# Performance work log

Hardware: AMD Instinct MI355X
Metric: run time of the kernel (lower is better)

## Reference

```python
import jax, jax.numpy as jnp
import numpy as np

EPS = 1e-05
FACT = 2.0
REJECT_RATIO = 1.0


def setup_inputs() -> dict:
    key = jax.random.key(0)
    k1, k2 = jax.random.split(key)
    B, N = 8, 4096
    pc1 = jax.random.normal(k1, (B, 4, N), dtype=jnp.float32)
    pc2 = jax.random.normal(k2, (B, 4, N), dtype=jnp.float32)
    # homogeneous coordinates: last row = 1
    pc1 = pc1.at[:, 3, :].set(1.0)
    pc2 = pc2.at[:, 3, :].set(1.0)
    return {"pc1": pc1, "pc2": pc2}


def _rot_to_quat(R):
    # standard rotation-matrix -> quaternion (w, x, y, z)
    r00, r11, r22 = R[0, 0], R[1, 1], R[2, 2]
    qw = 0.5 * jnp.sqrt(jnp.maximum(1e-12, 1.0 + r00 + r11 + r22))
    qx = 0.5 * jnp.sqrt(jnp.maximum(0.0, 1.0 + r00 - r11 - r22))
    qy = 0.5 * jnp.sqrt(jnp.maximum(0.0, 1.0 - r00 + r11 - r22))
    qz = 0.5 * jnp.sqrt(jnp.maximum(0.0, 1.0 - r00 - r11 + r22))
    qx = jnp.where(R[2, 1] - R[1, 2] < 0, -qx, qx)
    qy = jnp.where(R[0, 2] - R[2, 0] < 0, -qy, qy)
    qz = jnp.where(R[1, 0] - R[0, 1] < 0, -qz, qz)
    return jnp.stack([qw, qx, qy, qz])


def _normalize_rotmat(R):
    # operates on COLUMNS, like the torch code (R[:, 2] etc.)
    z = R[:, 2] / jnp.linalg.norm(R[:, 2])
    y = R[:, 1]
    x = jnp.cross(y, z)
    x = x / jnp.linalg.norm(x)
    y = jnp.cross(z, x)
    return jnp.stack([x, y, z], axis=1)


def _norm_tf(pc):
    # T = diag(1/std) @ [I | -mean]  (std is unbiased, as torch.std)
    std = jnp.std(pc[:3, :], axis=1, ddof=1)
    mean = jnp.mean(pc[:3, :], axis=1)
    T = jnp.zeros((4, 4), dtype=pc.dtype)
    T = T.at[jnp.arange(3), jnp.arange(3)].set(1.0 / std)
    T = T.at[:3, 3].set(-mean / std)
    T = T.at[3, 3].set(1.0)
    return T


def _per_sample(pc1, pc2):
    # ---- soft_knn: pairwise squared distance over xyz ----
    p1, p2 = pc1[:3], pc2[:3]  # (3, N)
    d = ((p1 ** 2).sum(0)[:, None]
         - 2.0 * jnp.einsum('dn,dm->nm', p1, p2)
         + (p2 ** 2).sum(0)[None, :])            # (N1, N2)
    W = jax.nn.softmax(FACT / jnp.clip(d, EPS, None), axis=1)
    pc_nearest = pc2 @ W.T                        # (4, N1) soft-gathered points

    # ---- soft_outlier_rejection ----
    dist = jnp.linalg.norm(pc1 - pc_nearest, axis=0)
    filt = jax.nn.sigmoid((dist - dist.mean() * REJECT_RATIO - EPS) * -1e10)

    # ---- dlt(pc1, pc_nearest, filt) ----
    T2 = _norm_tf(pc_nearest)
    pc2n = T2 @ pc_nearest
    T1 = _norm_tf(pc1)
    pc1n = T1 @ pc1

    mask = (filt > 0.5).astype(pc1.dtype)         # hard inlier mask (sigmoid slope 1e10)
    N = pc1.shape[1]
    a = pc1n.T                                    # (N, 4)
    z4 = jnp.zeros((N, 4), dtype=pc1.dtype)
    row0 = jnp.concatenate([z4, -pc2n[2][:, None] * a, pc2n[1][:, None] * a], axis=1)
    row1 = jnp.concatenate([pc2n[2][:, None] * a, z4, -pc2n[0][:, None] * a], axis=1)
    M = (jnp.stack([row0, row1], axis=1) * mask[:, None, None]).reshape(2 * N, 12)

    _, _, Vh = jnp.linalg.svd(M, full_matrices=False)
    p = Vh[-1]                                    # null-space vector (12,)
    p = jnp.where(p[10] < 0, -p, p)
    p = p / jnp.sqrt(p[8] ** 2 + p[9] ** 2 + p[10] ** 2)

    T = jnp.zeros((4, 4), dtype=pc1.dtype)
    T = T.at[:3, :].set(p.reshape(3, 4)).at[3, 3].set(1.0)
    T = jnp.linalg.inv(T2) @ T @ T1
    R = _normalize_rotmat(T[:3, :3])
    T = T.at[:3, :3].set(R)
    return T, _rot_to_quat(R), T[:3, 3]


def reference(pc1, pc2):
    T, q, t = jax.vmap(_per_sample)(pc1, pc2)
    return T, q, t
```

## Files before the change

kernel.cpp:

```cpp
#include <hip/hip_runtime.h>
#include <math.h>

#define NPTS 4096
#define EPSC 1e-5f
#define F2C (2.0f*1.44269504088896340736f)

#if __has_builtin(__builtin_amdgcn_exp2f)
#define FEXP2 __builtin_amdgcn_exp2f
#else
#define FEXP2(x) __expf((x)*0.6931471805599453f)
#endif

#define IDX(i,j) ((i)*((i)+1)/2 + (j))

__global__ void __launch_bounds__(256) k_soft(const float* __restrict__ pc1,
                                              const float* __restrict__ pc2,
                                              float4* __restrict__ part4,
                                              float* __restrict__ partZ){
  constexpr int CHN = 256, NC = 16;
  int bid = blockIdx.x;
  int chunk = bid & (NC-1), rb = (bid/NC) & 15, b = bid/(NC*16);

  __shared__ float4 sp[CHN];
  {
    const float* p2 = pc2 + (size_t)b*4*NPTS + chunk*CHN;
    for (int m = threadIdx.x; m < CHN; m += 256){
      float x = p2[m], y = p2[m+NPTS], z = p2[m+2*NPTS];
      sp[m] = make_float4(x, y, z, x*x + y*y + z*z);
    }
  }
  __syncthreads();

  int n = rb*256 + threadIdx.x;
  const float* p1 = pc1 + (size_t)b*4*NPTS + n;
  float x1 = p1[0], y1 = p1[NPTS], z1 = p1[2*NPTS];
  float q1 = x1*x1 + y1*y1 + z1*z1;
  float mx = -2.f*x1, my = -2.f*y1, mz = -2.f*z1;

  float4 c0 = sp[0];
  float d0 = fmaf(mx,c0.x, fmaf(my,c0.y, fmaf(mz,c0.z, c0.w + q1)));
  float m_ = F2C * __builtin_amdgcn_rcpf(fmaxf(d0, EPSC));
  float L = 1.f, Ax = c0.x, Ay = c0.y, Az = c0.z;

  #pragma unroll 8
  for (int mm=1; mm<CHN; ++mm){
    float4 c = sp[mm];
    float d = fmaf(mx,c.x, fmaf(my,c.y, fmaf(mz,c.z, c.w + q1)));
    float dinv = __builtin_amdgcn_rcpf(fmaxf(d, EPSC));
    float t = fmaf(F2C, dinv, -m_);
    if (__any(t > 0.f)){
      float tp = fmaxf(t, 0.f);
      float sc = FEXP2(-tp);
      L *= sc; Ax *= sc; Ay *= sc; Az *= sc;
      m_ += tp;
      t = fminf(t, 0.f);
    }
    float pe = FEXP2(t);
    L += pe;
    Ax = fmaf(pe,c.x,Ax); Ay = fmaf(pe,c.y,Ay); Az = fmaf(pe,c.z,Az);
  }
  size_t idx = (size_t)(b*NC + chunk)*NPTS + n;
  part4[idx] = make_float4(m_, L, Ax, Ay);
  partZ[idx] = Az;
}

__global__ void __launch_bounds__(256) k_mid(const float* __restrict__ pc1,
                                             const float4* __restrict__ part4,
                                             const float* __restrict__ partZ,
                                             float4* __restrict__ rowdat,
                                             float* __restrict__ psum13){
  constexpr int NC = 16;
  int b = blockIdx.x >> 4, rb = blockIdx.x & 15, t = threadIdx.x;
  int n = rb*256 + t;
  float4 f[NC]; float zz[NC];
  #pragma unroll
  for (int c=0;c<NC;c++){
    size_t idx = (size_t)(b*NC + c)*NPTS + n;
    f[c]  = part4[idx];
    zz[c] = partZ[idx];
  }
  float S = f[0].x;
  #pragma unroll
  for (int c=1;c<NC;c++) S = fmaxf(S, f[c].x);
  float L=0.f, Ax=0.f, Ay=0.f, Az=0.f;
  #pragma unroll
  for (int c=0;c<NC;c++){
    float w = FEXP2(f[c].x - S);
    L  = fmaf(w, f[c].y, L);
    Ax = fmaf(w, f[c].z, Ax);
    Ay = fmaf(w, f[c].w, Ay);
    Az = fmaf(w, zz[c],  Az);
  }
  float inv = 1.f/L;
  float px=Ax*inv, py=Ay*inv, pz=Az*inv;
  const float* p1 = pc1 + (size_t)b*4*NPTS + n;
  float x1=p1[0], y1=p1[NPTS], z1=p1[2*NPTS];
  float dx=x1-px, dy=y1-py, dz=z1-pz;
  float dd=sqrtf(dx*dx+dy*dy+dz*dz);
  rowdat[(size_t)b*NPTS + n] = make_float4(px,py,pz,dd);

  float acc[13]={x1,y1,z1,x1*x1,y1*y1,z1*z1,px,py,pz,px*px,py*py,pz*pz,dd};
  __shared__ float red[4][13];
  int lane = t & 63, wv = t >> 6;
  #pragma unroll
  for (int k=0;k<13;k++){
    float v = acc[k];
    v += __shfl_xor(v,32); v += __shfl_xor(v,16); v += __shfl_xor(v,8);
    v += __shfl_xor(v,4);  v += __shfl_xor(v,2);  v += __shfl_xor(v,1);
    if (lane==0) red[wv][k]=v;
  }
  __syncthreads();
  if (t<13)
    psum13[(size_t)blockIdx.x*13 + t] = red[0][t]+red[1][t]+red[2][t]+red[3][t];
}

__device__ __forceinline__ void stats_from_tot(const float* stot, float* sst){
  const float Nf = 4096.f, Nm1 = 4095.f;
  #pragma unroll
  for (int j=0;j<3;j++){
    float m  = stot[j]/Nf;
    float v  = (stot[3+j]-Nf*m*m)/Nm1;
    sst[j]=m; sst[3+j]=sqrtf(fmaxf(v,0.f));
    float m2 = stot[6+j]/Nf;
    float v2 = (stot[9+j]-Nf*m2*m2)/Nm1;
    sst[6+j]=m2; sst[9+j]=sqrtf(fmaxf(v2,0.f));
  }
  sst[12]=stot[12]/Nf;
}

__device__ __forceinline__ float elemA(const float* S, int i, int k){
  int bi=i>>2, bj=k>>2;
  int ii=i&3, jj=k&3;
  int lo = ii<jj?ii:jj, hi = ii<jj?jj:ii;
  int pe = 4*lo - ((lo*(lo-1))>>1) + (hi-lo);
  int w;
  if (bi==bj) w = (bi==2)?30:0;
  else {
    int blo = bi<bj?bi:bj, bhi = bi<bj?bj:bi;
    if (blo==0 && bhi==1) return 0.f;
    w = (blo==0)?10:20;
  }
  return S[w+pe];
}

__global__ void __launch_bounds__(1024) k_fin(const float* __restrict__ pc1,
                                              const float4* __restrict__ rowdat,
                                              const float* __restrict__ psum13,
                                              float* __restrict__ out){
  int b = blockIdx.x, t = threadIdx.x;
  int lane = t & 63, wv = t >> 6;

  __shared__ float stot[13];
  __shared__ float sst[13];
  __shared__ float red40[16][40];
  __shared__ float SS[40];

  if (t<13){
    float s=0.f;
    #pragma unroll
    for (int i=0;i<16;i++) s += psum13[(size_t)(b*16+i)*13 + t];
    stot[t]=s;
  }
  __syncthreads();
  if (t==0) stats_from_tot(stot, sst);
  __syncthreads();

  float i1x=1.f/sst[3], i1y=1.f/sst[4], i1z=1.f/sst[5];
  float t1x=-sst[0]/sst[3], t1y=-sst[1]/sst[4], t1z=-sst[2]/sst[5];
  float i2x=1.f/sst[9], i2y=1.f/sst[10], i2z=1.f/sst[11];
  float t2x=-sst[6]/sst[9], t2y=-sst[7]/sst[10], t2z=-sst[8]/sst[11];
  float meanD=sst[12];

  float acc[40];
  #pragma unroll
  for (int k=0;k<40;k++) acc[k]=0.f;
  #pragma unroll
  for (int i=0;i<4;i++){
    int n = i*1024 + t;
    const float* p1 = pc1 + (size_t)b*4*NPTS + n;
    float X1=fmaf(p1[0],i1x,t1x), Y1=fmaf(p1[NPTS],i1y,t1y), Z1=fmaf(p1[2*NPTS],i1z,t1z);
    float4 rd = rowdat[(size_t)b*NPTS + n];
    float X2=fmaf(rd.x,i2x,t2x);
    float Y2=fmaf(rd.y,i2y,t2y);
    float Z2=fmaf(rd.z,i2z,t2z);
    float zthr = (rd.w - meanD) - EPSC;
    float msk = (zthr < 0.f) ? 1.f : 0.f;
    float tz = msk*Z2;
    float wA = tz*Z2, wB = -tz*X2, wC = -tz*Y2;
    float wD = msk*fmaf(X2,X2,Y2*Y2);
    float ee[10]={X1*X1, X1*Y1, X1*Z1, X1, Y1*Y1, Y1*Z1, Y1, Z1*Z1, Z1, 1.f};
    #pragma unroll
    for (int j=0;j<10;j++){
      acc[j]    = fmaf(wA,ee[j],acc[j]);
      acc[10+j] = fmaf(wB,ee[j],acc[10+j]);
      acc[20+j] = fmaf(wC,ee[j],acc[20+j]);
      acc[30+j] = fmaf(wD,ee[j],acc[30+j]);
    }
  }
  #pragma unroll
  for (int k=0;k<40;k++){
    float v=acc[k];
    v+=__shfl_xor(v,32); v+=__shfl_xor(v,16); v+=__shfl_xor(v,8);
    v+=__shfl_xor(v,4);  v+=__shfl_xor(v,2);  v+=__shfl_xor(v,1);
    if(lane==0) red40[wv][k]=v;
  }
  __syncthreads();
  if (t<40){
    float s=0.f;
    #pragma unroll
    for (int w=0;w<16;w++) s += red40[w][t];
    SS[t]=s;
  }
  __syncthreads();

  if (t<64){
    float a[78];
    #pragma unroll
    for (int i=0;i<12;i++)
      #pragma unroll
      for (int j=0;j<=i;j++)
        a[IDX(i,j)] = elemA(SS,i,j);
    {
      float tr=0.f;
      #pragma unroll
      for (int i=0;i<12;i++) tr += a[IDX(i,i)];
      float eps = 1e-5f * tr * (1.f/12.f);
      #pragma unroll
      for (int i=0;i<12;i++) a[IDX(i,i)] += eps;
    }
    #pragma unroll
    for (int j=0;j<12;j++){
      float s = a[IDX(j,j)];
      #pragma unroll
      for (int k=0;k<j;k++) s = fmaf(-a[IDX(j,k)], a[IDX(j,k)], s);
      float d = sqrtf(fmaxf(s, 1e-30f));
      a[IDX(j,j)] = d;
      float dinv = __builtin_amdgcn_rcpf(d);
      #pragma unroll
      for (int i=j+1;i<12;i++){
        float s2 = a[IDX(i,j)];
        #pragma unroll
        for (int k=0;k<j;k++) s2 = fmaf(-a[IDX(i,k)], a[IDX(j,k)], s2);
        a[IDX(i,j)] = s2 * dinv;
      }
    }
    float y[12], Brow[12];
    #pragma unroll
    for (int i=0;i<12;i++){
      float s = (i==t) ? 1.f : 0.f;
      #pragma unroll
      for (int k=0;k<i;k++) s = fmaf(-a[IDX(i,k)], y[k], s);
      y[i] = s * __builtin_amdgcn_rcpf(a[IDX(i,i)]);
    }
    #pragma unroll
    for (int i=11;i>=0;i--){
      float s = y[i];
      #pragma unroll
      for (int k=11;k>i;k--) s = fmaf(-a[IDX(k,i)], Brow[k], s);
      Brow[i] = s * __builtin_amdgcn_rcpf(a[IDX(i,i)]);
    }
    {
      float mxv = 0.f;
      #pragma unroll
      for (int i=0;i<12;i++) mxv = fmaxf(mxv, fabsf(Brow[i]));
      mxv = fmaxf(mxv, __shfl_xor(mxv,1)); mxv = fmaxf(mxv, __shfl_xor(mxv,2));
      mxv = fmaxf(mxv, __shfl_xor(mxv,4)); mxv = fmaxf(mxv, __shfl_xor(mxv,8));
      float sc = __builtin_amdgcn_rcpf(mxv);
      #pragma unroll
      for (int i=0;i<12;i++) Brow[i] *= sc;
    }
    #pragma unroll
    for (int rep=0; rep<2; ++rep){
      float nr[12];
      #pragma unroll
      for (int i=0;i<12;i++) nr[i]=0.f;
      #pragma unroll
      for (int k=0;k<12;k++){
        float bjk = Brow[k];
        #pragma unroll
        for (int m2=0;m2<12;m2++){
          float bkm = __shfl(Brow[m2], k);
          nr[m2] = fmaf(bjk, bkm, nr[m2]);
        }
      }
      float mxv = 0.f;
      #pragma unroll
      for (int i=0;i<12;i++) mxv = fmaxf(mxv, fabsf(nr[i]));
      mxv = fmaxf(mxv, __shfl_xor(mxv,1)); mxv = fmaxf(mxv, __shfl_xor(mxv,2));
      mxv = fmaxf(mxv, __shfl_xor(mxv,4)); mxv = fmaxf(mxv, __shfl_xor(mxv,8));
      float sc = __builtin_amdgcn_rcpf(mxv);
      #pragma unroll
      for (int i=0;i<12;i++) Brow[i] = nr[i]*sc;
    }
    float v = 0.f;
    #pragma unroll
    for (int i=0;i<12;i++) v += Brow[i];
    #pragma unroll
    for (int it=0; it<14; ++it){
      float w = 0.f;
      #pragma unroll
      for (int k=0;k<12;k++) w = fmaf(Brow[k], __shfl(v,k), w);
      float nn = w*w;
      nn += __shfl_xor(nn,1); nn += __shfl_xor(nn,2);
      nn += __shfl_xor(nn,4); nn += __shfl_xor(nn,8);
      v = w * rsqrtf(nn);
    }
    float pvf[12];
    #pragma unroll
    for (int i=0;i<12;i++) pvf[i] = __shfl(v, i);

    if (t==0){
      double pv[12];
      #pragma unroll
      for (int i=0;i<12;i++) pv[i]=(double)pvf[i];
      if (pv[10]<0.0){
        #pragma unroll
        for (int i=0;i<12;i++) pv[i]=-pv[i];
      }
      double nrm = sqrt(pv[8]*pv[8]+pv[9]*pv[9]+pv[10]*pv[10]);
      #pragma unroll
      for (int i=0;i<12;i++) pv[i]/=nrm;
      double m1[3]={sst[0],sst[1],sst[2]}, sd1[3]={sst[3],sst[4],sst[5]};
      double m2[3]={sst[6],sst[7],sst[8]}, sd2[3]={sst[9],sst[10],sst[11]};
      double Td[3][4]={{pv[0],pv[1],pv[2],pv[3]},
                       {pv[4],pv[5],pv[6],pv[7]},
                       {pv[8],pv[9],pv[10],pv[11]}};
      double F[3][4];
      for (int i=0;i<3;i++){
        double b3 = Td[i][3];
        for (int j=0;j<3;j++){
          F[i][j] = sd2[i]*(Td[i][j]/sd1[j]);
          b3 += Td[i][j]*(-m1[j]/sd1[j]);
        }
        F[i][3] = sd2[i]*b3 + m2[i];
      }
      double zx=F[0][2],zy=F[1][2],zz2=F[2][2];
      double zn=sqrt(zx*zx+zy*zy+zz2*zz2);
      zx/=zn; zy/=zn; zz2/=zn;
      double yx=F[0][1],yy=F[1][1],yz=F[2][1];
      double xx=yy*zz2-yz*zy, xy=yz*zx-yx*zz2, xz=yx*zy-yy*zx;
      double xn=sqrt(xx*xx+xy*xy+xz*xz);
      xx/=xn; xy/=xn; xz/=xn;
      double y2x=zy*xz-zz2*xy, y2y=zz2*xx-zx*xz, y2z=zx*xy-zy*xx;
      double R00=xx,R01=y2x,R02=zx;
      double R10=xy,R11=y2y,R12=zy;
      double R20=xz,R21=y2z,R22=zz2;
      float* oT = out + b*16;
      oT[0]=(float)R00; oT[1]=(float)R01; oT[2]=(float)R02; oT[3]=(float)F[0][3];
      oT[4]=(float)R10; oT[5]=(float)R11; oT[6]=(float)R12; oT[7]=(float)F[1][3];
      oT[8]=(float)R20; oT[9]=(float)R21; oT[10]=(float)R22; oT[11]=(float)F[2][3];
      oT[12]=0.f; oT[13]=0.f; oT[14]=0.f; oT[15]=1.f;
      double qw=0.5*sqrt(fmax(1e-12, 1.0+R00+R11+R22));
      double qx=0.5*sqrt(fmax(0.0, 1.0+R00-R11-R22));
      double qy=0.5*sqrt(fmax(0.0, 1.0-R00+R11-R22));
      double qz=0.5*sqrt(fmax(0.0, 1.0-R00-R11+R22));
      if (R21-R12<0.0) qx=-qx;
      if (R02-R20<0.0) qy=-qy;
      if (R10-R01<0.0) qz=-qz;
      float* oQ = out + 128 + b*4;
      oQ[0]=(float)qw; oQ[1]=(float)qx; oQ[2]=(float)qy; oQ[3]=(float)qz;
      float* ot3 = out + 160 + b*3;
      ot3[0]=(float)F[0][3]; ot3[1]=(float)F[1][3]; ot3[2]=(float)F[2][3];
    }
  }
}

extern "C" void kernel_launch(void* const* d_in, const int* in_sizes, int n_in,
                              void* d_out, int out_size, void* d_ws, size_t ws_size,
                              hipStream_t stream) {
  const float* pc1 = (const float*)d_in[0];
  const float* pc2 = (const float*)d_in[1];
  float* out  = (float*)d_out;
  float* ws   = (float*)d_ws;

  float4* part4  = (float4*)ws;
  float*  partZ  = ws + 2097152;
  float4* rowdat = (float4*)(ws + 2097152 + 524288);
  float*  psum13 = ws + 2097152 + 524288 + 131072;

  hipLaunchKernelGGL(k_soft, dim3(2048), dim3(256),  0, stream, pc1, pc2, part4, partZ);
  hipLaunchKernelGGL(k_mid,  dim3(128),  dim3(256),  0, stream, pc1, part4, partZ, rowdat, psum13);
  hipLaunchKernelGGL(k_fin,  dim3(8),    dim3(1024), 0, stream, pc1, rowdat, psum13, out);
}
```

Before: 169.1 us.

## Fuse split-softmax merge into k_soft via last-block atomic counter

Drops the separate k_mid kernel. The last of the 16 chunk blocks for each row block, detected with an atomic counter plus threadfences, merges the partial softmax states and writes the soft-nearest point and distance. The 13 statistics reduction moves into k_fin, which now re-reads pc1 and rowdat. This saves one kernel launch and its global round trip, at the cost of a memset, atomics and a serial tail in the last blocks.

```diff
diff --git a/kernel.cpp b/kernel.cpp
--- a/kernel.cpp
+++ b/kernel.cpp
@@ -15,8 +15,10 @@
 
 __global__ void __launch_bounds__(256) k_soft(const float* __restrict__ pc1,
                                               const float* __restrict__ pc2,
-                                              float4* __restrict__ part4,
-                                              float* __restrict__ partZ){
+                                              float* __restrict__ partM,
+                                              float4* __restrict__ partV,
+                                              float4* __restrict__ rowdat,
+                                              unsigned int* __restrict__ ctr){
   constexpr int CHN = 256, NC = 16;
   int bid = blockIdx.x;
   int chunk = bid & (NC-1), rb = (bid/NC) & 15, b = bid/(NC*16);
@@ -59,59 +61,42 @@
     L += pe;
     Ax = fmaf(pe,c.x,Ax); Ay = fmaf(pe,c.y,Ay); Az = fmaf(pe,c.z,Az);
   }
-  size_t idx = (size_t)(b*NC + chunk)*NPTS + n;
-  part4[idx] = make_float4(m_, L, Ax, Ay);
-  partZ[idx] = Az;
-}
-
-__global__ void __launch_bounds__(256) k_mid(const float* __restrict__ pc1,
-                                             const float4* __restrict__ part4,
-                                             const float* __restrict__ partZ,
-                                             float4* __restrict__ rowdat,
-                                             float* __restrict__ psum13){
-  constexpr int NC = 16;
-  int b = blockIdx.x >> 4, rb = blockIdx.x & 15, t = threadIdx.x;
-  int n = rb*256 + t;
-  float4 f[NC]; float zz[NC];
+  size_t base = (size_t)(b*NC)*NPTS + n;
+  partM[base + (size_t)chunk*NPTS] = m_;
+  partV[base + (size_t)chunk*NPTS] = make_float4(L, Ax, Ay, Az);
+
+  __threadfence();
+  __syncthreads();
+  __shared__ int lastBlk;
+  if (threadIdx.x==0){
+    unsigned int old = atomicAdd(&ctr[b*16+rb], 1u);
+    lastBlk = (old == NC-1);
+  }
+  __syncthreads();
+  if (!lastBlk) return;
+  __threadfence();
+
+  float mc[NC];
+  #pragma unroll
+  for (int c=0;c<NC;c++) mc[c] = partM[base + (size_t)c*NPTS];
+  float M = mc[0];
+  #pragma unroll
+  for (int c=1;c<NC;c++) M = fmaxf(M, mc[c]);
+  float Lm=0.f, Axm=0.f, Aym=0.f, Azm=0.f;
   #pragma unroll
   for (int c=0;c<NC;c++){
-    size_t idx = (size_t)(b*NC + c)*NPTS + n;
-    f[c]  = part4[idx];
-    zz[c] = partZ[idx];
-  }
-  float S = f[0].x;
-  #pragma unroll
-  for (int c=1;c<NC;c++) S = fmaxf(S, f[c].x);
-  float L=0.f, Ax=0.f, Ay=0.f, Az=0.f;
-  #pragma unroll
-  for (int c=0;c<NC;c++){
-    float w = FEXP2(f[c].x - S);
-    L  = fmaf(w, f[c].y, L);
-    Ax = fmaf(w, f[c].z, Ax);
-    Ay = fmaf(w, f[c].w, Ay);
-    Az = fmaf(w, zz[c],  Az);
-  }
-  float inv = 1.f/L;
-  float px=Ax*inv, py=Ay*inv, pz=Az*inv;
-  const float* p1 = pc1 + (size_t)b*4*NPTS + n;
-  float x1=p1[0], y1=p1[NPTS], z1=p1[2*NPTS];
+    float4 v = partV[base + (size_t)c*NPTS];
+    float w = FEXP2(mc[c]-M);
+    Lm  = fmaf(w, v.x, Lm);
+    Axm = fmaf(w, v.y, Axm);
+    Aym = fmaf(w, v.z, Aym);
+    Azm = fmaf(w, v.w, Azm);
+  }
+  float inv = 1.f/Lm;
+  float px=Axm*inv, py=Aym*inv, pz=Azm*inv;
   float dx=x1-px, dy=y1-py, dz=z1-pz;
   float dd=sqrtf(dx*dx+dy*dy+dz*dz);
   rowdat[(size_t)b*NPTS + n] = make_float4(px,py,pz,dd);
-
-  float acc[13]={x1,y1,z1,x1*x1,y1*y1,z1*z1,px,py,pz,px*px,py*py,pz*pz,dd};
-  __shared__ float red[4][13];
-  int lane = t & 63, wv = t >> 6;
-  #pragma unroll
-  for (int k=0;k<13;k++){
-    float v = acc[k];
-    v += __shfl_xor(v,32); v += __shfl_xor(v,16); v += __shfl_xor(v,8);
-    v += __shfl_xor(v,4);  v += __shfl_xor(v,2);  v += __shfl_xor(v,1);
-    if (lane==0) red[wv][k]=v;
-  }
-  __syncthreads();
-  if (t<13)
-    psum13[(size_t)blockIdx.x*13 + t] = red[0][t]+red[1][t]+red[2][t]+red[3][t];
 }
 
 __device__ __forceinline__ void stats_from_tot(const float* stot, float* sst){
@@ -145,20 +130,43 @@
 
 __global__ void __launch_bounds__(1024) k_fin(const float* __restrict__ pc1,
                                               const float4* __restrict__ rowdat,
-                                              const float* __restrict__ psum13,
                                               float* __restrict__ out){
   int b = blockIdx.x, t = threadIdx.x;
   int lane = t & 63, wv = t >> 6;
 
+  __shared__ float red13[16][13];
   __shared__ float stot[13];
   __shared__ float sst[13];
   __shared__ float red40[16][40];
   __shared__ float SS[40];
 
+  float acc13[13];
+  #pragma unroll
+  for (int k=0;k<13;k++) acc13[k]=0.f;
+  #pragma unroll
+  for (int i=0;i<4;i++){
+    int n = i*1024 + t;
+    const float* p1 = pc1 + (size_t)b*4*NPTS + n;
+    float x1=p1[0], y1=p1[NPTS], z1=p1[2*NPTS];
+    float4 rd = rowdat[(size_t)b*NPTS + n];
+    acc13[0]+=x1;      acc13[1]+=y1;      acc13[2]+=z1;
+    acc13[3]+=x1*x1;   acc13[4]+=y1*y1;   acc13[5]+=z1*z1;
+    acc13[6]+=rd.x;    acc13[7]+=rd.y;    acc13[8]+=rd.z;
+    acc13[9]+=rd.x*rd.x; acc13[10]+=rd.y*rd.y; acc13[11]+=rd.z*rd.z;
+    acc13[12]+=rd.w;
+  }
+  #pragma unroll
+  for (int k=0;k<13;k++){
+    float v = acc13[k];
+    v += __shfl_xor(v,32); v += __shfl_xor(v,16); v += __shfl_xor(v,8);
+    v += __shfl_xor(v,4);  v += __shfl_xor(v,2);  v += __shfl_xor(v,1);
+    if (lane==0) red13[wv][k]=v;
+  }
+  __syncthreads();
   if (t<13){
     float s=0.f;
     #pragma unroll
-    for (int i=0;i<16;i++) s += psum13[(size_t)(b*16+i)*13 + t];
+    for (int w=0;w<16;w++) s += red13[w][t];
     stot[t]=s;
   }
   __syncthreads();
@@ -373,12 +381,14 @@
   float* out  = (float*)d_out;
   float* ws   = (float*)d_ws;
 
-  float4* part4  = (float4*)ws;
-  float*  partZ  = ws + 2097152;
-  float4* rowdat = (float4*)(ws + 2097152 + 524288);
-  float*  psum13 = ws + 2097152 + 524288 + 131072;
-
-  hipLaunchKernelGGL(k_soft, dim3(2048), dim3(256),  0, stream, pc1, pc2, part4, partZ);
-  hipLaunchKernelGGL(k_mid,  dim3(128),  dim3(256),  0, stream, pc1, part4, partZ, rowdat, psum13);
-  hipLaunchKernelGGL(k_fin,  dim3(8),    dim3(1024), 0, stream, pc1, rowdat, psum13, out);
-}
+  float*        partM  = ws;
+  float4*       partV  = (float4*)(ws + 524288);
+  float4*       rowdat = (float4*)(ws + 524288 + 2097152);
+  unsigned int* ctr    = (unsigned int*)(ws + 524288 + 2097152 + 131072);
+
+  hipMemsetAsync((void*)ctr, 0, 128*sizeof(unsigned int), stream);
+  hipLaunchKernelGGL(k_soft, dim3(2048), dim3(256),  0, stream,
+                     pc1, pc2, partM, partV, rowdat, ctr);
+  hipLaunchKernelGGL(k_fin,  dim3(8),    dim3(1024), 0, stream,
+                     pc1, rowdat, out);
+}
```

Result: slower. 358.9 us (+112.2%).
